# Kernel optimization log

Measured on AMD Instinct MI355X. Metric: run time of the kernel, lower is better.

Reference implementation:

```python
import jax, jax.numpy as jnp
import numpy as np

E = 768   # embedding_dim
D = 64    # head_dim
B = 8
S = 2048


def setup_inputs() -> dict:
    key = jax.random.key(0)
    k1, k2, k3, k4 = jax.random.split(key, 4)
    inputs = jax.random.normal(k1, (B, S, E), dtype=jnp.float32)
    # causal mask: 1 where attending allowed, 0 elsewhere (masked_fill where ==0)
    attention_mask = jnp.tril(jnp.ones((S, S), dtype=jnp.int32))[None, :, :]
    Q = jax.random.normal(k2, (E, D), dtype=jnp.float32) * 0.01
    K = jax.random.normal(k3, (E, D), dtype=jnp.float32) * 0.01
    V = jax.random.normal(k4, (E, D), dtype=jnp.float32) * 0.01
    return {"inputs": inputs, "attention_mask": attention_mask, "Q": Q, "K": K, "V": V}


def reference(inputs, attention_mask, Q, K, V):
    scale = 1.0 / np.sqrt(D).astype(np.float32)
    q = inputs @ Q          # [B,S,D]
    k = inputs @ K          # [B,S,D]
    v = inputs @ V          # [B,S,D]
    w = jnp.einsum('bqd,bkd->bqk', q, k) * scale   # [B,S,S]
    w = jnp.where(attention_mask == 0, -jnp.inf, w)
    attn = jax.nn.softmax(w, axis=-1)              # [B,S,S]
    states = attn @ v                              # [B,S,D] (dropout p=0.0 is identity)
    return states
```

## Files before the change

kernel.cpp:

```cpp
#include <hip/hip_runtime.h>
#include <cstdint>

#define B_ 8
#define S_ 2048
#define E_ 768
#define D_ 64
#define NSPLIT 4
#define SEGLEN (S_ / NSPLIT)
#define ROWS (B_ * S_)

typedef unsigned short ushort_t;
typedef __attribute__((ext_vector_type(8))) short s16x8;
typedef __attribute__((ext_vector_type(4))) float f32x4;

__device__ inline ushort_t f2bf(float f) {
  unsigned int x = __float_as_uint(f);
  return (ushort_t)((x + 0x7fffu + ((x >> 16) & 1u)) >> 16);
}

__device__ inline unsigned int pkbf(float hi, float lo) {
  return __builtin_amdgcn_perm(__float_as_uint(hi) + 0x8000u,
                               __float_as_uint(lo) + 0x8000u, 0x07060302u);
}

__device__ inline void async16(const void* g, void* l) {
  __builtin_amdgcn_global_load_lds(
      (const __attribute__((address_space(1))) unsigned int*)g,
      (__attribute__((address_space(3))) unsigned int*)l, 16, 0, 0);
}

__global__ __launch_bounds__(256) void wt_kernel(
    const float* __restrict__ Wq, const float* __restrict__ Wk,
    const float* __restrict__ Wv, ushort_t* __restrict__ wt) {
  const int mat = blockIdx.y;
  const int e = blockIdx.x * 4 + (threadIdx.x >> 6);
  const int d = threadIdx.x & 63;
  const float* W = (mat == 0) ? Wq : ((mat == 1) ? Wk : Wv);
  wt[(long)(mat * 64 + d) * E_ + e] = f2bf(W[(long)e * D_ + d]);
}

__global__ __launch_bounds__(512) void qkv_mfma(
    const float* __restrict__ in, const ushort_t* __restrict__ wt,
    ushort_t* __restrict__ qb, ushort_t* __restrict__ kb,
    ushort_t* __restrict__ vtb) {
  const int tid = threadIdx.x;
  const int w = tid >> 6;
  const int L = tid & 63;
  const int c = L & 15;
  const int q = L >> 4;
  const int row0 = blockIdx.x * 64;

  __shared__ float Alds[2][64][64];
  __shared__ ushort_t Blds[2][192][64];

  const int ar0 = w * 8 + (L >> 4);
  const int ar1 = ar0 + 4;
  const int asl = L & 15;
  const float* asrc0 = in + (long)(row0 + ar0) * E_ + ((asl ^ (ar0 & 15)) << 2);
  const float* asrc1 = in + (long)(row0 + ar1) * E_ + ((asl ^ (ar1 & 15)) << 2);
  const int bsl = L & 7;
  const ushort_t* bsrc[3];
#pragma unroll
  for (int jj = 0; jj < 3; ++jj) {
    const int br = w * 24 + jj * 8 + (L >> 3);
    bsrc[jj] = wt + (long)br * E_ + ((bsl ^ (br & 7)) << 3);
  }
  float* ad[2] = {&Alds[0][w * 8][0], &Alds[1][w * 8][0]};
  ushort_t* bd[2] = {&Blds[0][w * 24][0], &Blds[1][w * 24][0]};

  const int mloc = w & 3;
  const int nbase = (w >> 2) * 6;
  const int ra = mloc * 16 + c;
  const int offA00 = ra * 256 + ((2 * q + 0) ^ c) * 16;
  const int offA01 = ra * 256 + ((2 * q + 1) ^ c) * 16;
  const int offA10 = ra * 256 + ((8 + 2 * q + 0) ^ c) * 16;
  const int offA11 = ra * 256 + ((8 + 2 * q + 1) ^ c) * 16;
  int offB0[6], offB1[6];
#pragma unroll
  for (int t = 0; t < 6; ++t) {
    const int n = (nbase + t) * 16 + c;
    offB0[t] = n * 128 + ((q + 0) ^ (c & 7)) * 16;
    offB1[t] = n * 128 + ((q + 4) ^ (c & 7)) * 16;
  }
  const char* Abase = (const char*)&Alds[0][0][0];
  const char* Bbase = (const char*)&Blds[0][0][0];

  f32x4 acc[6];
#pragma unroll
  for (int n = 0; n < 6; ++n) acc[n] = (f32x4){0.f, 0.f, 0.f, 0.f};

  async16(asrc0, ad[0]);
  async16(asrc1, ad[0] + 4 * 64);
#pragma unroll
  for (int jj = 0; jj < 3; ++jj) async16(bsrc[jj], bd[0] + jj * 8 * 64);
  asrc0 += 64; asrc1 += 64;
#pragma unroll
  for (int jj = 0; jj < 3; ++jj) bsrc[jj] += 64;

  for (int it = 0; it < E_ / 64; ++it) {
    const int b = it & 1;
    __syncthreads();
    if (it + 1 < E_ / 64) {
      const int nb = 1 - b;
      async16(asrc0, ad[nb]);
      async16(asrc1, ad[nb] + 4 * 64);
#pragma unroll
      for (int jj = 0; jj < 3; ++jj) async16(bsrc[jj], bd[nb] + jj * 8 * 64);
      asrc0 += 64; asrc1 += 64;
#pragma unroll
      for (int jj = 0; jj < 3; ++jj) bsrc[jj] += 64;
    }
    const char* Ab = Abase + b * 16384;
    const char* Bb = Bbase + b * 24576;
    const float4 a00 = *(const float4*)(Ab + offA00);
    const float4 a01 = *(const float4*)(Ab + offA01);
    const float4 a10 = *(const float4*)(Ab + offA10);
    const float4 a11 = *(const float4*)(Ab + offA11);
    union { s16x8 v; unsigned int u[4]; } af0, af1;
    af0.u[0] = pkbf(a00.y, a00.x);
    af0.u[1] = pkbf(a00.w, a00.z);
    af0.u[2] = pkbf(a01.y, a01.x);
    af0.u[3] = pkbf(a01.w, a01.z);
    af1.u[0] = pkbf(a10.y, a10.x);
    af1.u[1] = pkbf(a10.w, a10.z);
    af1.u[2] = pkbf(a11.y, a11.x);
    af1.u[3] = pkbf(a11.w, a11.z);
#pragma unroll
    for (int t = 0; t < 6; ++t) {
      const s16x8 bf0 = *(const s16x8*)(Bb + offB0[t]);
      const s16x8 bf1 = *(const s16x8*)(Bb + offB1[t]);
      acc[t] = __builtin_amdgcn_mfma_f32_16x16x32_bf16(af0.v, bf0, acc[t], 0, 0, 0);
      acc[t] = __builtin_amdgcn_mfma_f32_16x16x32_bf16(af1.v, bf1, acc[t], 0, 0, 0);
    }
  }

  const float qscale = 0.125f * 1.44269504088896340736f;
  const int row0w = row0 + mloc * 16;
  const int b_ = row0w >> 11;
  const int srow = row0w & (S_ - 1);
#pragma unroll
  for (int n = 0; n < 6; ++n) {
    const int gn = nbase + n;
    const int mat = gn >> 2;
    const int d0 = (gn & 3) * 16 + c;
#pragma unroll
    for (int reg = 0; reg < 4; ++reg) {
      const int m = q * 4 + reg;
      const float x = acc[n][reg];
      if (mat == 0) {
        qb[(long)(row0w + m) * D_ + d0] = f2bf(x * qscale);
      } else if (mat == 1) {
        kb[(long)(row0w + m) * D_ + d0] = f2bf(x);
      } else {
        vtb[(long)b_ * D_ * S_ + (long)d0 * S_ + srow + m] = f2bf(x);
      }
    }
  }
}

__global__ __launch_bounds__(256) void attn_mfma(
    const ushort_t* __restrict__ qb, const ushort_t* __restrict__ kb,
    const ushort_t* __restrict__ vtb, float* __restrict__ op,
    float* __restrict__ lw) {
  const int task = blockIdx.x;
  const int batch = task / 80;
  const int r = task % 80;
  int seg, qi;
  if (r < 32)      { seg = 0; qi = r; }
  else if (r < 56) { seg = 1; qi = r - 24; }
  else if (r < 72) { seg = 2; qi = r - 40; }
  else             { seg = 3; qi = r - 48; }
  const int qb0 = qi * 64;
  const int j0 = seg * SEGLEN;
  const int jmax = min(j0 + SEGLEN, qb0 + 64);
  const int ntiles = (jmax - j0) >> 6;

  const int w = threadIdx.x >> 6;
  const int L = threadIdx.x & 63;
  const int col = L & 15;
  const int quad = L >> 4;

  __shared__ ushort_t Kl[2][64][64];
  __shared__ ushort_t Vl[2][64][64];
  __shared__ ushort_t Pl[4][16][72];

  const ushort_t* kbb = kb + (long)batch * S_ * D_;
  const ushort_t* vbb = vtb + (long)batch * D_ * S_;

  const int rl = (w << 4) + (L >> 3);
  const int gsw = (L & 7) ^ (rl & 7);
  const ushort_t* ksrc = kbb + ((long)(j0 + rl) << 6) + gsw * 8;
  const ushort_t* vsrc = vbb + (long)rl * S_ + j0 + gsw * 8;
  ushort_t* kdst[2] = {&Kl[0][w * 16][0], &Kl[1][w * 16][0]};
  ushort_t* vdst[2] = {&Vl[0][w * 16][0], &Vl[1][w * 16][0]};

  const int s0 = ((quad ^ (col & 7)) * 16);

  const ushort_t* qrow = qb + ((long)(batch * S_ + qb0 + w * 16 + col) * D_);
  const s16x8 qf0 = *(const s16x8*)(qrow + quad * 8);
  const s16x8 qf1 = *(const s16x8*)(qrow + 32 + quad * 8);

  f32x4 O[4];
#pragma unroll
  for (int t = 0; t < 4; ++t) O[t] = (f32x4){0.f, 0.f, 0.f, 0.f};
  float l[4] = {0.f, 0.f, 0.f, 0.f};

  async16(ksrc, kdst[0]);
  async16(ksrc + 512, kdst[0] + 512);
  async16(vsrc, vdst[0]);
  async16(vsrc + 8 * S_, vdst[0] + 512);
  ksrc += 64 * 64; vsrc += 64;

  for (int i = 0; i < ntiles; ++i) {
    const int b = i & 1;
    const int kt = j0 + i * 64;
    __syncthreads();
    if (i + 1 < ntiles) {
      const int nb = 1 - b;
      async16(ksrc, kdst[nb]);
      async16(ksrc + 512, kdst[nb] + 512);
      async16(vsrc, vdst[nb]);
      async16(vsrc + 8 * S_, vdst[nb] + 512);
      ksrc += 64 * 64; vsrc += 64;
    }
    const char* Kb = (const char*)&Kl[b][0][0];
    const char* Vb = (const char*)&Vl[b][0][0];

    f32x4 S[4];
    __builtin_amdgcn_s_setprio(1);
#pragma unroll
    for (int t = 0; t < 4; ++t) {
      const s16x8 kf0 = *(const s16x8*)(Kb + (t * 16 + col) * 128 + s0);
      const s16x8 kf1 = *(const s16x8*)(Kb + (t * 16 + col) * 128 + (s0 ^ 64));
      f32x4 z = (f32x4){0.f, 0.f, 0.f, 0.f};
      z = __builtin_amdgcn_mfma_f32_16x16x32_bf16(qf0, kf0, z, 0, 0, 0);
      S[t] = __builtin_amdgcn_mfma_f32_16x16x32_bf16(qf1, kf1, z, 0, 0, 0);
    }
    __builtin_amdgcn_s_setprio(0);
    if (kt + 64 > qb0) {
#pragma unroll
      for (int t = 0; t < 4; ++t) {
        const int colg = kt + t * 16 + col;
#pragma unroll
        for (int reg = 0; reg < 4; ++reg) {
          const int rowg = qb0 + w * 16 + quad * 4 + reg;
          if (colg > rowg) S[t][reg] = -1e30f;
        }
      }
    }
    float P[4][4];
#pragma unroll
    for (int t = 0; t < 4; ++t)
#pragma unroll
      for (int reg = 0; reg < 4; ++reg) {
        P[t][reg] = exp2f(S[t][reg]);
        l[reg] += P[t][reg];
      }
#pragma unroll
    for (int t = 0; t < 4; ++t)
#pragma unroll
      for (int reg = 0; reg < 4; ++reg)
        Pl[w][quad * 4 + reg][t * 16 + col] = f2bf(P[t][reg]);
    const s16x8 p0 = *(const s16x8*)&Pl[w][col][quad * 8];
    const s16x8 p1 = *(const s16x8*)&Pl[w][col][32 + quad * 8];
    __builtin_amdgcn_s_setprio(1);
#pragma unroll
    for (int t = 0; t < 4; ++t) {
      const s16x8 vf0 = *(const s16x8*)(Vb + (t * 16 + col) * 128 + s0);
      const s16x8 vf1 = *(const s16x8*)(Vb + (t * 16 + col) * 128 + (s0 ^ 64));
      O[t] = __builtin_amdgcn_mfma_f32_16x16x32_bf16(p0, vf0, O[t], 0, 0, 0);
      O[t] = __builtin_amdgcn_mfma_f32_16x16x32_bf16(p1, vf1, O[t], 0, 0, 0);
    }
    __builtin_amdgcn_s_setprio(0);
  }
#pragma unroll
  for (int off = 1; off < 16; off <<= 1)
#pragma unroll
    for (int reg = 0; reg < 4; ++reg)
      l[reg] += __shfl_xor(l[reg], off);

  const int growbase = batch * S_ + qb0 + w * 16;
#pragma unroll
  for (int t = 0; t < 4; ++t)
#pragma unroll
    for (int reg = 0; reg < 4; ++reg)
      op[((long)seg * ROWS + growbase + quad * 4 + reg) * D_ + t * 16 + col] =
          O[t][reg];
  if (col == 0) {
#pragma unroll
    for (int reg = 0; reg < 4; ++reg)
      lw[(long)seg * ROWS + growbase + quad * 4 + reg] = l[reg];
  }
}

__global__ __launch_bounds__(256) void attn_combine(
    const float* __restrict__ op, const float* __restrict__ lw,
    float* __restrict__ out) {
  const int t = threadIdx.x;
  const int d = t & 63;
  const int g = blockIdx.x * 4 + (t >> 6);
  const int s_q = g & (S_ - 1);
  float osum = 0.f, lsum = 0.f;
#pragma unroll
  for (int s = 0; s < NSPLIT; ++s) {
    if (s_q >= s * SEGLEN) {
      osum += op[((long)s * ROWS + g) * D_ + d];
      lsum += lw[(long)s * ROWS + g];
    }
  }
  out[(long)g * D_ + d] = osum / lsum;
}

extern "C" void kernel_launch(void* const* d_in, const int* in_sizes, int n_in,
                              void* d_out, int out_size, void* d_ws, size_t ws_size,
                              hipStream_t stream) {
  const float* in = (const float*)d_in[0];
  const float* Wq = (const float*)d_in[2];
  const float* Wk = (const float*)d_in[3];
  const float* Wv = (const float*)d_in[4];
  float* out = (float*)d_out;

  ushort_t* qbuf = (ushort_t*)d_ws;
  ushort_t* kbuf = qbuf + (long)ROWS * D_;
  ushort_t* vtb = kbuf + (long)ROWS * D_;
  float* op = (float*)(vtb + (long)ROWS * D_);
  float* lw = op + (long)NSPLIT * ROWS * D_;
  ushort_t* wt = (ushort_t*)(lw + (long)NSPLIT * ROWS);

  wt_kernel<<<dim3(E_ / 4, 3), 256, 0, stream>>>(Wq, Wk, Wv, wt);
  qkv_mfma<<<ROWS / 64, 512, 0, stream>>>(in, wt, qbuf, kbuf, vtb);
  attn_mfma<<<640, 256, 0, stream>>>(qbuf, kbuf, vtb, op, lw);
  attn_combine<<<(ROWS * D_) / 256, 256, 0, stream>>>(op, lw, out);
}
```

Before: 134.5 us.

## Triple-buffer QKV projection loads with explicit waitcnt and vectorize combine kernel

The QKV projection GEMM moves from a double-buffered LDS pipeline with a full __syncthreads per iteration to a three-stage ring. Loads are issued two stages ahead, and partial s_waitcnt vmcnt plus raw s_barrier let global loads overlap more compute. The combine kernel now uses float4 loads and stores with one reciprocal per row. The third stage raises LDS use to about 120KB per block, which may limit occupancy, and the hand-written waitcnt counts must match the number of async loads issued.

```diff
diff --git a/kernel.cpp b/kernel.cpp
--- a/kernel.cpp
+++ b/kernel.cpp
@@ -50,8 +50,8 @@
   const int q = L >> 4;
   const int row0 = blockIdx.x * 64;
 
-  __shared__ float Alds[2][64][64];
-  __shared__ ushort_t Blds[2][192][64];
+  __shared__ float Alds[3][64][64];
+  __shared__ ushort_t Blds[3][192][64];
 
   const int ar0 = w * 8 + (L >> 4);
   const int ar1 = ar0 + 4;
@@ -65,8 +65,8 @@
     const int br = w * 24 + jj * 8 + (L >> 3);
     bsrc[jj] = wt + (long)br * E_ + ((bsl ^ (br & 7)) << 3);
   }
-  float* ad[2] = {&Alds[0][w * 8][0], &Alds[1][w * 8][0]};
-  ushort_t* bd[2] = {&Blds[0][w * 24][0], &Blds[1][w * 24][0]};
+  char* adb = (char*)&Alds[0][w * 8][0];
+  char* bdb = (char*)&Blds[0][w * 24][0];
 
   const int mloc = w & 3;
   const int nbase = (w >> 2) * 6;
@@ -89,50 +89,66 @@
 #pragma unroll
   for (int n = 0; n < 6; ++n) acc[n] = (f32x4){0.f, 0.f, 0.f, 0.f};
 
-  async16(asrc0, ad[0]);
-  async16(asrc1, ad[0] + 4 * 64);
-#pragma unroll
-  for (int jj = 0; jj < 3; ++jj) async16(bsrc[jj], bd[0] + jj * 8 * 64);
-  asrc0 += 64; asrc1 += 64;
-#pragma unroll
-  for (int jj = 0; jj < 3; ++jj) bsrc[jj] += 64;
-
-  for (int it = 0; it < E_ / 64; ++it) {
-    const int b = it & 1;
-    __syncthreads();
-    if (it + 1 < E_ / 64) {
-      const int nb = 1 - b;
-      async16(asrc0, ad[nb]);
-      async16(asrc1, ad[nb] + 4 * 64);
-#pragma unroll
-      for (int jj = 0; jj < 3; ++jj) async16(bsrc[jj], bd[nb] + jj * 8 * 64);
-      asrc0 += 64; asrc1 += 64;
-#pragma unroll
-      for (int jj = 0; jj < 3; ++jj) bsrc[jj] += 64;
-    }
-    const char* Ab = Abase + b * 16384;
-    const char* Bb = Bbase + b * 24576;
-    const float4 a00 = *(const float4*)(Ab + offA00);
-    const float4 a01 = *(const float4*)(Ab + offA01);
-    const float4 a10 = *(const float4*)(Ab + offA10);
-    const float4 a11 = *(const float4*)(Ab + offA11);
-    union { s16x8 v; unsigned int u[4]; } af0, af1;
-    af0.u[0] = pkbf(a00.y, a00.x);
-    af0.u[1] = pkbf(a00.w, a00.z);
-    af0.u[2] = pkbf(a01.y, a01.x);
-    af0.u[3] = pkbf(a01.w, a01.z);
-    af1.u[0] = pkbf(a10.y, a10.x);
-    af1.u[1] = pkbf(a10.w, a10.z);
-    af1.u[2] = pkbf(a11.y, a11.x);
-    af1.u[3] = pkbf(a11.w, a11.z);
-#pragma unroll
-    for (int t = 0; t < 6; ++t) {
-      const s16x8 bf0 = *(const s16x8*)(Bb + offB0[t]);
-      const s16x8 bf1 = *(const s16x8*)(Bb + offB1[t]);
-      acc[t] = __builtin_amdgcn_mfma_f32_16x16x32_bf16(af0.v, bf0, acc[t], 0, 0, 0);
-      acc[t] = __builtin_amdgcn_mfma_f32_16x16x32_bf16(af1.v, bf1, acc[t], 0, 0, 0);
-    }
-  }
+#define QSTAGE(IDX)                                                          \
+  {                                                                          \
+    const int m3_ = (IDX) % 3;                                               \
+    async16(asrc0, adb + m3_ * 16384);                                       \
+    async16(asrc1, adb + m3_ * 16384 + 1024);                                \
+    _Pragma("unroll")                                                        \
+    for (int jj = 0; jj < 3; ++jj)                                           \
+      async16(bsrc[jj], bdb + m3_ * 24576 + jj * 1024);                      \
+    asrc0 += 64; asrc1 += 64;                                                \
+    _Pragma("unroll")                                                        \
+    for (int jj = 0; jj < 3; ++jj) bsrc[jj] += 64;                           \
+    __builtin_amdgcn_sched_barrier(0);                                       \
+  }
+
+#define QCOMP(IT)                                                            \
+  {                                                                          \
+    const int m3_ = (IT) % 3;                                                \
+    const char* Ab = Abase + m3_ * 16384;                                    \
+    const char* Bb = Bbase + m3_ * 24576;                                    \
+    const float4 a00 = *(const float4*)(Ab + offA00);                        \
+    const float4 a01 = *(const float4*)(Ab + offA01);                        \
+    const float4 a10 = *(const float4*)(Ab + offA10);                        \
+    const float4 a11 = *(const float4*)(Ab + offA11);                        \
+    union { s16x8 v; unsigned int u[4]; } af0, af1;                          \
+    af0.u[0] = pkbf(a00.y, a00.x);                                           \
+    af0.u[1] = pkbf(a00.w, a00.z);                                           \
+    af0.u[2] = pkbf(a01.y, a01.x);                                           \
+    af0.u[3] = pkbf(a01.w, a01.z);                                           \
+    af1.u[0] = pkbf(a10.y, a10.x);                                           \
+    af1.u[1] = pkbf(a10.w, a10.z);                                           \
+    af1.u[2] = pkbf(a11.y, a11.x);                                           \
+    af1.u[3] = pkbf(a11.w, a11.z);                                           \
+    _Pragma("unroll")                                                        \
+    for (int t = 0; t < 6; ++t) {                                            \
+      const s16x8 bf0 = *(const s16x8*)(Bb + offB0[t]);                      \
+      const s16x8 bf1 = *(const s16x8*)(Bb + offB1[t]);                      \
+      acc[t] =                                                               \
+          __builtin_amdgcn_mfma_f32_16x16x32_bf16(af0.v, bf0, acc[t], 0, 0, 0);\
+      acc[t] =                                                               \
+          __builtin_amdgcn_mfma_f32_16x16x32_bf16(af1.v, bf1, acc[t], 0, 0, 0);\
+    }                                                                        \
+  }
+
+  QSTAGE(0);
+  QSTAGE(1);
+
+  for (int it = 0; it < 11; ++it) {
+    asm volatile("s_waitcnt vmcnt(5)" ::: "memory");
+    __builtin_amdgcn_s_barrier();
+    __builtin_amdgcn_sched_barrier(0);
+    if (it < 10) QSTAGE(it + 2);
+    QCOMP(it);
+  }
+  asm volatile("s_waitcnt vmcnt(0)" ::: "memory");
+  __builtin_amdgcn_s_barrier();
+  __builtin_amdgcn_sched_barrier(0);
+  QCOMP(11);
+
+#undef QSTAGE
+#undef QCOMP
 
   const float qscale = 0.125f * 1.44269504088896340736f;
   const int row0w = row0 + mloc * 16;
@@ -297,18 +313,22 @@
     const float* __restrict__ op, const float* __restrict__ lw,
     float* __restrict__ out) {
   const int t = threadIdx.x;
-  const int d = t & 63;
-  const int g = blockIdx.x * 4 + (t >> 6);
+  const int d4 = (t & 15) * 4;
+  const int g = blockIdx.x * 16 + (t >> 4);
   const int s_q = g & (S_ - 1);
-  float osum = 0.f, lsum = 0.f;
+  float4 osum = {0.f, 0.f, 0.f, 0.f};
+  float lsum = 0.f;
 #pragma unroll
   for (int s = 0; s < NSPLIT; ++s) {
     if (s_q >= s * SEGLEN) {
-      osum += op[((long)s * ROWS + g) * D_ + d];
+      const float4 v = *(const float4*)&op[((long)s * ROWS + g) * D_ + d4];
+      osum.x += v.x; osum.y += v.y; osum.z += v.z; osum.w += v.w;
       lsum += lw[(long)s * ROWS + g];
     }
   }
-  out[(long)g * D_ + d] = osum / lsum;
+  const float inv = 1.0f / lsum;
+  float4 r = {osum.x * inv, osum.y * inv, osum.z * inv, osum.w * inv};
+  *(float4*)&out[(long)g * D_ + d4] = r;
 }
 
 extern "C" void kernel_launch(void* const* d_in, const int* in_sizes, int n_in,
@@ -330,5 +350,5 @@
   wt_kernel<<<dim3(E_ / 4, 3), 256, 0, stream>>>(Wq, Wk, Wv, wt);
   qkv_mfma<<<ROWS / 64, 512, 0, stream>>>(in, wt, qbuf, kbuf, vtb);
   attn_mfma<<<640, 256, 0, stream>>>(qbuf, kbuf, vtb, op, lw);
-  attn_combine<<<(ROWS * D_) / 256, 256, 0, stream>>>(op, lw, out);
-}
+  attn_combine<<<ROWS / 16, 256, 0, stream>>>(op, lw, out);
+}
```

After: 136.9 us. Within noise of the previous version (+1.8%).
